# Optimization experiments

Measured on AMD Instinct MI355X. Metric: run time of the kernel, lower is better.

Reference implementation:

```python
import jax, jax.numpy as jnp
import numpy as np

L, B, E, H = 1024, 8, 1024, 16


def setup_inputs() -> dict:
    key = jax.random.key(0)
    k1, k2, k3, k4, k5 = jax.random.split(key, 5)
    scale = 1.0 / np.sqrt(E)
    return {
        "x": jax.random.normal(k1, (L, B, E), dtype=jnp.float32),
        "in_proj_weight": jax.random.normal(k2, (3 * E, E), dtype=jnp.float32) * scale,
        "in_proj_bias": jax.random.normal(k3, (3 * E,), dtype=jnp.float32) * 0.01,
        "out_proj_weight": jax.random.normal(k4, (E, E), dtype=jnp.float32) * scale,
        "out_proj_bias": jax.random.normal(k5, (E,), dtype=jnp.float32) * 0.01,
        "num_heads": H,
    }


def reference(x, in_proj_weight, in_proj_bias, out_proj_weight, out_proj_bias, num_heads):
    # x: [L, B, E] (tgt_len, batch, embed_dim), self-attention path of
    # multi_head_attention_func (no masks, no bias_k/v, no add_zero_attn,
    # dropout_p=0 / eval mode).
    Lq, Bq, Eq = x.shape
    hd = Eq // num_heads
    scaling = float(hd) ** -0.5
    # fused qkv projection: linear(x, in_proj_weight, in_proj_bias).chunk(3)
    qkv = x @ in_proj_weight.T + in_proj_bias  # [L, B, 3E]
    q, k, v = jnp.split(qkv, 3, axis=-1)
    q = q * scaling
    def to_heads(t):  # [L, B, E] -> [B*H, L, hd]
        return t.reshape(Lq, Bq * num_heads, hd).transpose(1, 0, 2)
    q, k, v = to_heads(q), to_heads(k), to_heads(v)
    # explicit QK^T -> softmax -> PV (naive attention, as in the source)
    scores = jnp.einsum('bqd,bkd->bqk', q, k)      # [B*H, L, L]
    attn = jax.nn.softmax(scores, axis=-1)
    out = jnp.einsum('bqk,bkd->bqd', attn, v)      # [B*H, L, hd]
    out = out.transpose(1, 0, 2).reshape(Lq, Bq, Eq)
    out = out @ out_proj_weight.T + out_proj_bias  # [L, B, E]
    return out
```

## Files before the change

### kernel.cpp

```cpp
#include <hip/hip_runtime.h>

#define L_DIM 1024
#define B_DIM 8
#define E_DIM 1024
#define H_DIM 16
#define HD 64
#define BH_DIM (B_DIM * H_DIM)

typedef float f32x4 __attribute__((ext_vector_type(4)));
typedef _Float16 f16_t;
typedef f16_t f16x4 __attribute__((ext_vector_type(4)));
typedef f16_t f16x8 __attribute__((ext_vector_type(8)));

static __device__ __forceinline__ void gld16(const void* g, void* l) {
  __builtin_amdgcn_global_load_lds(
      (const __attribute__((address_space(1))) unsigned int*)g,
      (__attribute__((address_space(3))) unsigned int*)l, 16, 0, 0);
}

__global__ __launch_bounds__(256) void convert_f16(
    const float* __restrict__ x, const float* __restrict__ wi,
    const float* __restrict__ wo, f16_t* __restrict__ x16,
    f16_t* __restrict__ wi16, f16_t* __restrict__ wo16) {
  const int NX = (L_DIM * B_DIM * E_DIM) / 4;
  const int NWI = (3 * E_DIM * E_DIM) / 4;
  const int NWO = (E_DIM * E_DIM) / 4;
  const int total = NX + NWI + NWO;
  for (int i = blockIdx.x * blockDim.x + threadIdx.x; i < total;
       i += gridDim.x * blockDim.x) {
    const float4* src; f16_t* dst; int j;
    if (i < NX)            { src = (const float4*)x;  dst = x16;  j = i; }
    else if (i < NX + NWI) { src = (const float4*)wi; dst = wi16; j = i - NX; }
    else                   { src = (const float4*)wo; dst = wo16; j = i - NX - NWI; }
    const float4 v = src[j];
    f16x4 h = {(f16_t)v.x, (f16_t)v.y, (f16_t)v.z, (f16_t)v.w};
    *(f16x4*)(dst + (size_t)j * 4) = h;
  }
}


#define GQ_FENCE asm volatile("" ::: "memory")
#define GQ_BARRIER do { GQ_FENCE; __builtin_amdgcn_s_barrier(); GQ_FENCE; } while (0)
#define VMW(n) asm volatile("s_waitcnt vmcnt(" #n ")" ::: "memory")

static __device__ __forceinline__ const f16x8* fp16frag(
    const f16_t* tile, int r, int ks, int quad, int l16) {
  const int bo = (r * 128 + ks * 64 + quad * 16) ^ ((l16 & 7) << 4);
  return (const f16x8*)((const char*)tile + bo);
}

__global__ __launch_bounds__(256, 2) void gemm_qkv(
    const f16_t* __restrict__ A, const f16_t* __restrict__ B,
    const float* __restrict__ bias, f16_t* __restrict__ Oq,
    f16_t* __restrict__ Ok, f16_t* __restrict__ Ov) {
  constexpr int K = 1024;
  __shared__ __align__(16) f16_t As[2 * 8192];
  __shared__ __align__(16) f16_t Bs[2 * 8192];

  const int tid = threadIdx.x;
  const int lane = tid & 63;
  const int w = tid >> 6;
  const int wm = (w & 1) * 64;
  const int wn = (w >> 1) * 64;
  const int quad = lane >> 4;
  const int l16 = lane & 15;

  const int bid = blockIdx.x;
  const int xcd = bid & 7;
  const int idx = bid >> 3;
  const int tm = xcd * 8 + (idx & 7);
  const int tn = idx >> 3;
  const int m0 = tm * 128;
  const int n0 = tn * 128;

  const int r8 = tid >> 3;
  const int gsw = (tid & 7) ^ (r8 & 7);
  const f16_t* Abase = A + (size_t)(m0 + r8) * K + gsw * 8;
  const f16_t* Bbase = B + (size_t)(n0 + r8) * K + gsw * 8;

#define STAGE(kt, d) do {                                                    \
    _Pragma("unroll") for (int s_ = 0; s_ < 4; ++s_)                         \
      gld16(Abase + (size_t)s_ * 32 * K + (kt) * 64,                         \
            &As[(d) * 8192 + s_ * 2048 + tid * 8]);                          \
    _Pragma("unroll") for (int s_ = 0; s_ < 4; ++s_)                         \
      gld16(Bbase + (size_t)s_ * 32 * K + (kt) * 64,                         \
            &Bs[(d) * 8192 + s_ * 2048 + tid * 8]);                          \
  } while (0)

  f32x4 acc[4][4] = {};

  STAGE(0, 0);
  STAGE(1, 1);

#pragma unroll
  for (int t = 0; t < 16; ++t) {
    const int d = t & 1;
    VMW(8);
    GQ_BARRIER;

    f16x8 af[4][2], bf[4][2];
#pragma unroll
    for (int i = 0; i < 4; ++i)
#pragma unroll
      for (int ks = 0; ks < 2; ++ks) {
        af[i][ks] = *fp16frag(&As[d * 8192], wm + i * 16 + l16, ks, quad, l16);
        bf[i][ks] = *fp16frag(&Bs[d * 8192], wn + i * 16 + l16, ks, quad, l16);
      }

    __builtin_amdgcn_s_setprio(1);
#pragma unroll
    for (int i = 0; i < 4; ++i)
#pragma unroll
      for (int j = 0; j < 4; ++j)
#pragma unroll
        for (int ks = 0; ks < 2; ++ks)
          acc[i][j] = __builtin_amdgcn_mfma_f32_16x16x32_f16(
              af[i][ks], bf[j][ks], acc[i][j], 0, 0, 0);
    __builtin_amdgcn_s_setprio(0);

    GQ_BARRIER;
    const int kt2 = (t + 2 < 16) ? t + 2 : 15;
    STAGE(kt2, d);
  }

#pragma unroll
  for (int i = 0; i < 4; ++i) {
    const int mbase = m0 + wm + i * 16 + quad * 4;
#pragma unroll
    for (int c = 0; c < 4; ++c) {
      const int n = n0 + wn + c * 16 + l16;
      const float bv = bias[n];
      const int chunk = n >> 10;
      const int e = n & 1023;
      const int h = e >> 6;
      const int dd = e & 63;
#pragma unroll
      for (int r = 0; r < 4; ++r) {
        const int m = mbase + r;
        const int l = m >> 3, b = m & 7;
        const size_t idxo = ((size_t)(b * H_DIM + h) * L_DIM + l) * HD + dd;
        const float val = acc[i][c][r] + bv;
        if (chunk == 0)      Oq[idxo] = (f16_t)(val * 0.125f);
        else if (chunk == 1) Ok[idxo] = (f16_t)val;
        else                 Ov[idxo] = (f16_t)val;
      }
    }
  }
#undef STAGE
}

__global__ __launch_bounds__(256, 2) void gemm_out(
    const f16_t* __restrict__ A, const f16_t* __restrict__ B,
    const float* __restrict__ bias, float* __restrict__ O) {
  constexpr int K = 1024;
  __shared__ __align__(16) f16_t As[2 * 8192];
  __shared__ __align__(16) f16_t Bs[2 * 8192];

  const int tid = threadIdx.x;
  const int lane = tid & 63;
  const int w = tid >> 6;
  const int wm = (w & 1) * 64;
  const int wn = (w >> 1) * 64;
  const int quad = lane >> 4;
  const int l16 = lane & 15;

  const int bid = blockIdx.x;
  const int xcd = bid & 7;
  const int idx = bid >> 3;
  const int tm = xcd * 8 + (idx & 7);
  const int tn = idx >> 3;
  const int m0 = tm * 128;
  const int n0 = tn * 128;

  const int r8 = tid >> 3;
  const int gsw = (tid & 7) ^ (r8 & 7);
  const f16_t* Abase = A + (size_t)(m0 + r8) * K + gsw * 8;
  const f16_t* Bbase = B + (size_t)(n0 + r8) * K + gsw * 8;

#define STAGE(kt, d) do {                                                    \
    _Pragma("unroll") for (int s_ = 0; s_ < 4; ++s_)                         \
      gld16(Abase + (size_t)s_ * 32 * K + (kt) * 64,                         \
            &As[(d) * 8192 + s_ * 2048 + tid * 8]);                          \
    _Pragma("unroll") for (int s_ = 0; s_ < 4; ++s_)                         \
      gld16(Bbase + (size_t)s_ * 32 * K + (kt) * 64,                         \
            &Bs[(d) * 8192 + s_ * 2048 + tid * 8]);                          \
  } while (0)

  f32x4 acc[4][4] = {};

  STAGE(0, 0);
  STAGE(1, 1);

#pragma unroll
  for (int t = 0; t < 16; ++t) {
    const int d = t & 1;
    VMW(8);
    GQ_BARRIER;

    f16x8 af[4][2], bf[4][2];
#pragma unroll
    for (int i = 0; i < 4; ++i)
#pragma unroll
      for (int ks = 0; ks < 2; ++ks) {
        af[i][ks] = *fp16frag(&As[d * 8192], wm + i * 16 + l16, ks, quad, l16);
        bf[i][ks] = *fp16frag(&Bs[d * 8192], wn + i * 16 + l16, ks, quad, l16);
      }

    __builtin_amdgcn_s_setprio(1);
#pragma unroll
    for (int i = 0; i < 4; ++i)
#pragma unroll
      for (int j = 0; j < 4; ++j)
#pragma unroll
        for (int ks = 0; ks < 2; ++ks)
          acc[i][j] = __builtin_amdgcn_mfma_f32_16x16x32_f16(
              af[i][ks], bf[j][ks], acc[i][j], 0, 0, 0);
    __builtin_amdgcn_s_setprio(0);

    GQ_BARRIER;
    const int kt2 = (t + 2 < 16) ? t + 2 : 15;
    STAGE(kt2, d);
  }

#pragma unroll
  for (int i = 0; i < 4; ++i) {
    const int mbase = m0 + wm + i * 16 + quad * 4;
#pragma unroll
    for (int c = 0; c < 4; ++c) {
      const int n = n0 + wn + c * 16 + l16;
      const float bv = bias[n];
#pragma unroll
      for (int r = 0; r < 4; ++r) {
        const int m = mbase + r;
        O[(size_t)m * E_DIM + n] = acc[i][c][r] + bv;
      }
    }
  }
#undef STAGE
}

__global__ __launch_bounds__(256, 2) void attn_f16(
    const f16_t* __restrict__ Q, const f16_t* __restrict__ K,
    const f16_t* __restrict__ V, f16_t* __restrict__ O) {
  constexpr int KSTR = 70;
  __shared__ __align__(16) f16_t Ks[2][64 * KSTR];
  __shared__ __align__(16) f16_t Vs[2][64 * KSTR];
  __shared__ float Ls[4][64];

  const int tid = threadIdx.x;
  const int lane = tid & 63;
  const int w = tid >> 6;
  const int quad = lane >> 4;
  const int l16 = lane & 15;
  const int bh = blockIdx.y;
  const int q0 = blockIdx.x * 256 + w * 64;

  const f16_t* Qb = Q + (size_t)bh * L_DIM * HD;
  const f16_t* Kb = K + (size_t)bh * L_DIM * HD;
  const f16_t* Vb = V + (size_t)bh * L_DIM * HD;

  f16x8 qf[4][2];
#pragma unroll
  for (int nt = 0; nt < 4; ++nt)
#pragma unroll
    for (int kc = 0; kc < 2; ++kc)
      qf[nt][kc] = *(const f16x8*)(Qb + (size_t)(q0 + nt * 16 + l16) * HD + kc * 32 + quad * 8);

  f32x4 oacc[4][4] = {};
  float rsum[4] = {0.0f, 0.0f, 0.0f, 0.0f};

  const int sr = tid >> 3;
  const int sc8 = (tid & 7) * 8;
  const int va = tid & 31;
  const int vg = tid >> 5;
  const int rA = (l16 >> 2) * 8 + (l16 & 3);

  f16x8 kreg[2];
  unsigned int vd[8];

#define LOADKV(kt) do {                                                      \
    _Pragma("unroll") for (int rr_ = 0; rr_ < 2; ++rr_)                      \
      kreg[rr_] = *(const f16x8*)(Kb +                                       \
          (size_t)((kt) * 64 + sr + rr_ * 32) * HD + sc8);                   \
    const f16_t* vp_ = Vb + (size_t)((kt) * 64 + vg * 8) * HD + 2 * va;      \
    _Pragma("unroll") for (int i_ = 0; i_ < 8; ++i_)                         \
      vd[i_] = *(const unsigned int*)(vp_ + (size_t)i_ * HD);                \
  } while (0)

#define WRITEKV(nb) do {                                                     \
    _Pragma("unroll") for (int rr_ = 0; rr_ < 2; ++rr_)                      \
      *(f16x8*)&Ks[nb][(sr + rr_ * 32) * KSTR + sc8] = kreg[rr_];            \
    union { unsigned int u[4]; f16x8 v; } lo_, hi_;                          \
    _Pragma("unroll") for (int i_ = 0; i_ < 4; ++i_) {                       \
      lo_.u[i_] = (vd[2 * i_] & 0xffffu) | (vd[2 * i_ + 1] << 16);           \
      hi_.u[i_] = (vd[2 * i_] >> 16) | (vd[2 * i_ + 1] & 0xffff0000u);       \
    }                                                                        \
    *(f16x8*)&Vs[nb][(2 * va) * KSTR + vg * 8] = lo_.v;                      \
    *(f16x8*)&Vs[nb][(2 * va + 1) * KSTR + vg * 8] = hi_.v;                  \
  } while (0)

#define ATTN_SYNC do {                                                       \
    GQ_FENCE;                                                                \
    asm volatile("s_waitcnt lgkmcnt(0)" ::: "memory");                       \
    __builtin_amdgcn_s_barrier();                                            \
    GQ_FENCE;                                                                \
  } while (0)

#define ATTN_COMPUTE(nb) do {                                                \
    _Pragma("unroll") for (int c = 0; c < 2; ++c) {                          \
      f32x4 scv[2][4] = {};                                                  \
      __builtin_amdgcn_s_setprio(1);                                         \
      _Pragma("unroll") for (int h = 0; h < 2; ++h) {                        \
        const int row = c * 32 + h * 4 + rA;                                 \
        _Pragma("unroll") for (int kc = 0; kc < 2; ++kc) {                   \
          const f16x8 ka = *(const f16x8*)&Ks[nb][row * KSTR + kc * 32 + quad * 8]; \
          _Pragma("unroll") for (int nt = 0; nt < 4; ++nt)                   \
            scv[h][nt] = __builtin_amdgcn_mfma_f32_16x16x32_f16(             \
                ka, qf[nt][kc], scv[h][nt], 0, 0, 0);                        \
        }                                                                    \
      }                                                                      \
      __builtin_amdgcn_s_setprio(0);                                         \
      f16x8 pa[4];                                                           \
      _Pragma("unroll") for (int nt = 0; nt < 4; ++nt)                       \
        _Pragma("unroll") for (int h = 0; h < 2; ++h)                        \
          _Pragma("unroll") for (int r = 0; r < 4; ++r) {                    \
            const float e = __expf(scv[h][nt][r]);                           \
            rsum[nt] += e;                                                   \
            pa[nt][h * 4 + r] = (f16_t)e;                                    \
          }                                                                  \
      __builtin_amdgcn_s_setprio(1);                                         \
      _Pragma("unroll") for (int nd = 0; nd < 4; ++nd) {                     \
        const f16x8 vb = *(const f16x8*)&Vs[nb][(nd * 16 + l16) * KSTR + c * 32 + quad * 8]; \
        _Pragma("unroll") for (int nt = 0; nt < 4; ++nt)                     \
          oacc[nt][nd] = __builtin_amdgcn_mfma_f32_16x16x32_f16(             \
              pa[nt], vb, oacc[nt][nd], 0, 0, 0);                            \
      }                                                                      \
      __builtin_amdgcn_s_setprio(0);                                         \
    }                                                                        \
  } while (0)

  LOADKV(0);
  WRITEKV(0);
  LOADKV(1);
  ATTN_SYNC;

  for (int kt = 0; kt < 14; kt += 2) {
    ATTN_COMPUTE(0);
    WRITEKV(1);
    LOADKV(kt + 2);
    ATTN_SYNC;
    ATTN_COMPUTE(1);
    WRITEKV(0);
    LOADKV(kt + 3);
    ATTN_SYNC;
  }
  ATTN_COMPUTE(0);
  WRITEKV(1);
  ATTN_SYNC;
  ATTN_COMPUTE(1);

#undef LOADKV
#undef WRITEKV
#undef ATTN_SYNC
#undef ATTN_COMPUTE

#pragma unroll
  for (int nt = 0; nt < 4; ++nt) {
    float rs = rsum[nt];
    rs += __shfl_xor(rs, 16); rs += __shfl_xor(rs, 32);
    if (quad == 0) Ls[w][nt * 16 + l16] = rs;
  }
  asm volatile("s_waitcnt lgkmcnt(0)" ::: "memory");

  const int b = bh >> 4;
  const int h = bh & 15;
#pragma unroll
  for (int nt = 0; nt < 4; ++nt)
#pragma unroll
    for (int r = 0; r < 4; ++r) {
      const int ql = nt * 16 + quad * 4 + r;
      const float inv = 1.0f / Ls[w][ql];
      const int qrow = q0 + ql;
#pragma unroll
      for (int nd = 0; nd < 4; ++nd) {
        const int d = nd * 16 + l16;
        O[((size_t)qrow * B_DIM + b) * E_DIM + h * HD + d] = (f16_t)(oacc[nt][nd][r] * inv);
      }
    }
}

extern "C" void kernel_launch(void* const* d_in, const int* in_sizes, int n_in,
                              void* d_out, int out_size, void* d_ws, size_t ws_size,
                              hipStream_t stream) {
  const float* x     = (const float*)d_in[0];
  const float* w_in  = (const float*)d_in[1];
  const float* b_in  = (const float*)d_in[2];
  const float* w_out = (const float*)d_in[3];
  const float* b_out = (const float*)d_in[4];

  const size_t TS = (size_t)BH_DIM * L_DIM * HD;
  f16_t* q16  = (f16_t*)d_ws;
  f16_t* k16  = q16 + TS;
  f16_t* v16  = k16 + TS;
  f16_t* x16  = v16 + TS;
  f16_t* wi16 = x16 + TS;
  f16_t* wo16 = wi16 + (size_t)3 * E_DIM * E_DIM;
  f16_t* ao16 = x16;

  convert_f16<<<4096, 256, 0, stream>>>(x, w_in, w_out, x16, wi16, wo16);
  gemm_qkv<<<1536, 256, 0, stream>>>(x16, wi16, b_in, q16, k16, v16);
  attn_f16<<<dim3(4, 128), 256, 0, stream>>>(q16, k16, v16, ao16);
  gemm_out<<<512, 256, 0, stream>>>(ao16, wo16, b_out, (float*)d_out);
}
```

Measured before the change: 225.2 us.

## Split QKV GEMM into 256x256-tile Q/K kernel and 128-tile V kernel

Splits the QKV projection GEMM in two. The Q and K output columns go to a new 512-thread kernel with 256x256 tiles, an 8-phase software pipeline, a double buffer for both A and B, and barriers interleaved with the staging loads. The V columns stay on the original 128x128 kernel, offset to column 2048. Larger tiles raise arithmetic intensity and cut redundant global loads, at the cost of an extra kernel launch, more LDS and registers, and fewer blocks on the Q/K part.

```diff
diff --git a/kernel.cpp b/kernel.cpp
--- a/kernel.cpp
+++ b/kernel.cpp
@@ -38,10 +38,11 @@
   }
 }
 
-
 #define GQ_FENCE asm volatile("" ::: "memory")
 #define GQ_BARRIER do { GQ_FENCE; __builtin_amdgcn_s_barrier(); GQ_FENCE; } while (0)
 #define VMW(n) asm volatile("s_waitcnt vmcnt(" #n ")" ::: "memory")
+#define GQ_LGKM0 do { asm volatile("s_waitcnt lgkmcnt(0)" ::: "memory"); \
+                      __builtin_amdgcn_sched_barrier(0); } while (0)
 
 static __device__ __forceinline__ const f16x8* fp16frag(
     const f16_t* tile, int r, int ks, int quad, int l16) {
@@ -49,10 +50,126 @@
   return (const f16x8*)((const char*)tile + bo);
 }
 
-__global__ __launch_bounds__(256, 2) void gemm_qkv(
+
+#define STAGE_A2(d, ht, kt) do {                                             \
+    gld16(Asrc + (size_t)(ht) * (128 * 1024) + (kt) * 64,                    \
+          &As[(d) * 16384 + (ht) * 8192 + tid * 8]);                         \
+    gld16(Asrc + (size_t)(ht) * (128 * 1024) + 64 * 1024 + (kt) * 64,        \
+          &As[(d) * 16384 + (ht) * 8192 + 4096 + tid * 8]);                  \
+  } while (0)
+#define STAGE_B2(d, ht, kt) do {                                             \
+    gld16(Bsrc + (size_t)(ht) * (128 * 1024) + (kt) * 64,                    \
+          &Bs[(d) * 16384 + (ht) * 8192 + tid * 8]);                         \
+    gld16(Bsrc + (size_t)(ht) * (128 * 1024) + 64 * 1024 + (kt) * 64,        \
+          &Bs[(d) * 16384 + (ht) * 8192 + 4096 + tid * 8]);                  \
+  } while (0)
+
+#define PHA(d, g, STAGE_STMT, ENDWAIT) do {                                  \
+    f16x8 af_[2][2];                                                         \
+    _Pragma("unroll") for (int f_ = 0; f_ < 2; ++f_)                         \
+      _Pragma("unroll") for (int ks_ = 0; ks_ < 2; ++ks_)                    \
+        af_[f_][ks_] = *fp16frag(&As[(d) * 16384],                           \
+            wr * 128 + ((g) * 2 + f_) * 16 + l16, ks_, quad, l16);           \
+    if ((g) == 0) {                                                          \
+      _Pragma("unroll") for (int c_ = 0; c_ < 4; ++c_)                       \
+        _Pragma("unroll") for (int ks_ = 0; ks_ < 2; ++ks_)                  \
+          bf[c_][ks_] = *fp16frag(&Bs[(d) * 16384],                          \
+              wc * 64 + c_ * 16 + l16, ks_, quad, l16);                      \
+    }                                                                        \
+    STAGE_STMT;                                                              \
+    GQ_BARRIER;                                                              \
+    GQ_LGKM0;                                                                \
+    __builtin_amdgcn_s_setprio(1);                                           \
+    _Pragma("unroll") for (int f_ = 0; f_ < 2; ++f_)                         \
+      _Pragma("unroll") for (int c_ = 0; c_ < 4; ++c_)                       \
+        _Pragma("unroll") for (int ks_ = 0; ks_ < 2; ++ks_)                  \
+          acc[(g) * 2 + f_][c_] = __builtin_amdgcn_mfma_f32_16x16x32_f16(    \
+              af_[f_][ks_], bf[c_][ks_], acc[(g) * 2 + f_][c_], 0, 0, 0);    \
+    __builtin_amdgcn_s_setprio(0);                                           \
+    ENDWAIT;                                                                 \
+    GQ_BARRIER;                                                              \
+  } while (0)
+
+__global__ __launch_bounds__(512, 2) void gemm_qkv_a(
     const f16_t* __restrict__ A, const f16_t* __restrict__ B,
     const float* __restrict__ bias, f16_t* __restrict__ Oq,
     f16_t* __restrict__ Ok, f16_t* __restrict__ Ov) {
+  constexpr int K = 1024;
+  constexpr int NT = K / 64;
+  __shared__ __align__(16) f16_t As[2 * 16384];
+  __shared__ __align__(16) f16_t Bs[2 * 16384];
+
+  const int tid = threadIdx.x;
+  const int lane = tid & 63;
+  const int w = tid >> 6;
+  const int wr = w >> 2;
+  const int wc = w & 3;
+  const int quad = lane >> 4;
+  const int l16 = lane & 15;
+
+  const int bid = blockIdx.x;
+  const int xcd = bid & 7;
+  const int idx = bid >> 3;
+  const int tm = xcd * 4 + (idx & 3);
+  const int tn = idx >> 2;
+  const int m0 = tm * 256;
+  const int n0 = tn * 256;
+
+  const int srow = tid >> 3;
+  const int scol = ((tid & 7) ^ (srow & 7)) * 8;
+  const f16_t* Asrc = A + (size_t)(m0 + srow) * K + scol;
+  const f16_t* Bsrc = B + (size_t)(n0 + srow) * K + scol;
+
+  f32x4 acc[8][4] = {};
+  f16x8 bf[4][2];
+
+  STAGE_A2(0, 0, 0); STAGE_A2(0, 1, 0);
+  STAGE_B2(0, 0, 0); STAGE_B2(0, 1, 0);
+  STAGE_B2(1, 0, 1); STAGE_B2(1, 1, 1);
+  VMW(4);
+  GQ_BARRIER;
+
+  for (int it = 0; it < 8; ++it) {
+    const int t1 = 2 * it + 1;
+    const int ta = (2 * it + 2 < NT) ? 2 * it + 2 : NT - 1;
+    const int tb = (2 * it + 3 < NT) ? 2 * it + 3 : NT - 1;
+    PHA(0, 0, STAGE_A2(1, 0, t1), );
+    PHA(0, 1, STAGE_A2(1, 1, t1), );
+    PHA(0, 2, STAGE_B2(0, 0, ta), );
+    PHA(0, 3, STAGE_B2(0, 1, ta), VMW(4));
+    PHA(1, 0, STAGE_A2(0, 0, ta), );
+    PHA(1, 1, STAGE_A2(0, 1, ta), );
+    PHA(1, 2, STAGE_B2(1, 0, tb), );
+    PHA(1, 3, STAGE_B2(1, 1, tb), VMW(4));
+  }
+
+#pragma unroll
+  for (int i = 0; i < 8; ++i) {
+    const int mbase = m0 + wr * 128 + i * 16 + quad * 4;
+#pragma unroll
+    for (int c = 0; c < 4; ++c) {
+      const int n = n0 + wc * 64 + c * 16 + l16;
+      const float bv = bias[n];
+      const int chunk = n >> 10;
+      const int e = n & 1023;
+      const int h = e >> 6;
+      const int d = e & 63;
+#pragma unroll
+      for (int r = 0; r < 4; ++r) {
+        const int m = mbase + r;
+        const int l = m >> 3, b = m & 7;
+        const size_t idxo = ((size_t)(b * H_DIM + h) * L_DIM + l) * HD + d;
+        const float val = acc[i][c][r] + bv;
+        if (chunk == 0)      Oq[idxo] = (f16_t)(val * 0.125f);
+        else                 Ok[idxo] = (f16_t)val;
+      }
+    }
+  }
+}
+
+__global__ __launch_bounds__(256, 2) void gemm_qkv_b(
+    const f16_t* __restrict__ A, const f16_t* __restrict__ B,
+    const float* __restrict__ bias, f16_t* __restrict__ Ov) {
   constexpr int K = 1024;
   __shared__ __align__(16) f16_t As[2 * 8192];
   __shared__ __align__(16) f16_t Bs[2 * 8192];
@@ -71,7 +188,7 @@
   const int tm = xcd * 8 + (idx & 7);
   const int tn = idx >> 3;
   const int m0 = tm * 128;
-  const int n0 = tn * 128;
+  const int n0 = 2048 + tn * 128;
 
   const int r8 = tid >> 3;
   const int gsw = (tid & 7) ^ (r8 & 7);
@@ -130,7 +247,6 @@
     for (int c = 0; c < 4; ++c) {
       const int n = n0 + wn + c * 16 + l16;
       const float bv = bias[n];
-      const int chunk = n >> 10;
       const int e = n & 1023;
       const int h = e >> 6;
       const int dd = e & 63;
@@ -139,10 +255,7 @@
         const int m = mbase + r;
         const int l = m >> 3, b = m & 7;
         const size_t idxo = ((size_t)(b * H_DIM + h) * L_DIM + l) * HD + dd;
-        const float val = acc[i][c][r] + bv;
-        if (chunk == 0)      Oq[idxo] = (f16_t)(val * 0.125f);
-        else if (chunk == 1) Ok[idxo] = (f16_t)val;
-        else                 Ov[idxo] = (f16_t)val;
+        Ov[idxo] = (f16_t)(acc[i][c][r] + bv);
       }
     }
   }
@@ -408,7 +521,8 @@
   f16_t* ao16 = x16;
 
   convert_f16<<<4096, 256, 0, stream>>>(x, w_in, w_out, x16, wi16, wo16);
-  gemm_qkv<<<1536, 256, 0, stream>>>(x16, wi16, b_in, q16, k16, v16);
+  gemm_qkv_a<<<256, 512, 0, stream>>>(x16, wi16, b_in, q16, k16, v16);
+  gemm_qkv_b<<<512, 256, 0, stream>>>(x16, wi16, b_in, v16);
   attn_f16<<<dim3(4, 128), 256, 0, stream>>>(q16, k16, v16, ao16);
   gemm_out<<<512, 256, 0, stream>>>(ao16, wo16, b_out, (float*)d_out);
 }
```

Result: no change. 224.0 us (-0.5%).
